# Optimization experiments

Measured on AMD Instinct MI355X. Metric: run time of the kernel, lower is better.

The kernel has to match this reference:

```python
import jax, jax.numpy as jnp
import numpy as np

N_NODES = 100000
N_EDGES = 3200000
D_IN = 512
D_OUT = 256


def setup_inputs() -> dict:
    key = jax.random.key(0)
    k1, k2, k3, k4, k5 = jax.random.split(key, 5)
    x = jax.random.normal(k1, (N_NODES, D_IN), dtype=jnp.float32)
    edge_row = jax.random.randint(k2, (N_EDGES,), 0, N_NODES, dtype=jnp.int32)
    edge_col = jax.random.randint(k3, (N_EDGES,), 0, N_NODES, dtype=jnp.int32)
    edge_vals = jax.random.uniform(k4, (N_EDGES,), dtype=jnp.float32)
    # glorot uniform for W, zeros for bias (as in the torch module)
    init_range = float(np.sqrt(6.0 / (D_IN + D_OUT)))
    W = jax.random.uniform(k5, (D_IN, D_OUT), minval=-init_range, maxval=init_range, dtype=jnp.float32)
    b = jnp.zeros((D_OUT,), dtype=jnp.float32)
    return {"x": x, "edge_row": edge_row, "edge_col": edge_col,
            "edge_vals": edge_vals, "W": W, "b": b}


def reference(x, edge_row, edge_col, edge_vals, W, b):
    # dropout p=0 -> identity; feature transform
    pre_sup = x @ W                                   # [N, D_OUT]
    # SpMM: out[i] = sum_{e: row[e]==i} vals[e] * pre_sup[col[e]]
    gathered = pre_sup[edge_col] * edge_vals[:, None]  # [E, D_OUT]
    agg = jax.ops.segment_sum(gathered, edge_row, num_segments=N_NODES)
    out = agg + b
    # F.normalize(p=2, dim=0): L2-normalize each column over the node dim
    col_norm = jnp.sqrt(jnp.sum(out * out, axis=0, keepdims=True))
    out = out / jnp.maximum(col_norm, 1e-12)
    return jax.nn.softplus(out)
```

## Files before the change

### kernel.cpp

```cpp
#include <hip/hip_runtime.h>
#include <math.h>

#define N_NODES 100000
#define N_EDGES 3200000
#define D_IN 512
#define D_OUT 256
#define NBUK 391
#define LDA 40

typedef unsigned short ushort_t;
typedef unsigned int uint_t;

using f32x4 = __attribute__((ext_vector_type(4))) float;
using s16x8 = __attribute__((ext_vector_type(8))) short;

__device__ __forceinline__ ushort_t f2bf(float f) {
    union { float f; uint_t u; } v; v.f = f;
    uint_t r = v.u + 0x7FFFu + ((v.u >> 16) & 1u);
    return (ushort_t)(r >> 16);
}
__device__ __forceinline__ float bf2f(uint_t u) {
    union { uint_t u; float f; } v; v.u = u << 16;
    return v.f;
}

__global__ __launch_bounds__(256) void cvt_w(const float* __restrict__ W,
                                             ushort_t* __restrict__ Wt) {
    int idx = blockIdx.x * 256 + threadIdx.x;
    int k = idx >> 8, n = idx & 255;
    Wt[(size_t)n * D_IN + k] = f2bf(W[idx]);
}

__global__ __launch_bounds__(256) void gemm_xw(const float* __restrict__ X,
                                               const ushort_t* __restrict__ Wt,
                                               ushort_t* __restrict__ P) {
    __shared__ ushort_t As[128 * LDA];
    __shared__ ushort_t Bs[128 * LDA];
    const int tid = threadIdx.x;
    const int n0 = blockIdx.x * 128;
    const int m0 = blockIdx.y * 128;
    const int wave = tid >> 6, lane = tid & 63;
    const int quad = lane >> 4, r16 = lane & 15;
    const int wm = (wave >> 1) * 64, wn = (wave & 1) * 64;

    f32x4 acc[4][4] = {};

    for (int k0 = 0; k0 < D_IN; k0 += 32) {
#pragma unroll
        for (int it = 0; it < 2; ++it) {
            int f = tid + it * 256;
            int row = f >> 2, kc = (f & 3) * 8;
            int grow = m0 + row;
            s16x8 av = {};
            if (grow < N_NODES) {
                const float* xp = X + (size_t)grow * D_IN + k0 + kc;
                f32x4 v0 = *(const f32x4*)(xp);
                f32x4 v1 = *(const f32x4*)(xp + 4);
                av[0] = (short)f2bf(v0[0]); av[1] = (short)f2bf(v0[1]);
                av[2] = (short)f2bf(v0[2]); av[3] = (short)f2bf(v0[3]);
                av[4] = (short)f2bf(v1[0]); av[5] = (short)f2bf(v1[1]);
                av[6] = (short)f2bf(v1[2]); av[7] = (short)f2bf(v1[3]);
            }
            *(s16x8*)(&As[row * LDA + kc]) = av;
            s16x8 bv = *(const s16x8*)(Wt + (size_t)(n0 + row) * D_IN + k0 + kc);
            *(s16x8*)(&Bs[row * LDA + kc]) = bv;
        }
        __syncthreads();

        s16x8 a[4], b[4];
#pragma unroll
        for (int i = 0; i < 4; ++i)
            a[i] = *(const s16x8*)(&As[(wm + i * 16 + r16) * LDA + quad * 8]);
#pragma unroll
        for (int j = 0; j < 4; ++j)
            b[j] = *(const s16x8*)(&Bs[(wn + j * 16 + r16) * LDA + quad * 8]);
#pragma unroll
        for (int i = 0; i < 4; ++i)
#pragma unroll
            for (int j = 0; j < 4; ++j)
                acc[i][j] = __builtin_amdgcn_mfma_f32_16x16x32_bf16(a[i], b[j], acc[i][j], 0, 0, 0);
        __syncthreads();
    }

#pragma unroll
    for (int i = 0; i < 4; ++i) {
#pragma unroll
        for (int rr = 0; rr < 4; ++rr) {
            int grow = m0 + wm + i * 16 + quad * 4 + rr;
            if (grow >= N_NODES) continue;
#pragma unroll
            for (int j = 0; j < 4; ++j) {
                int gcol = n0 + wn + j * 16 + r16;
                P[(size_t)grow * D_OUT + gcol] = f2bf(acc[i][j][rr]);
            }
        }
    }
}

__global__ __launch_bounds__(256) void bhist(const int* __restrict__ erow,
                                             int* __restrict__ bcnt) {
    __shared__ int l[NBUK];
    for (int b = threadIdx.x; b < NBUK; b += 256) l[b] = 0;
    __syncthreads();
    int base = blockIdx.x * 4096;
#pragma unroll
    for (int i = 0; i < 16; ++i) {
        int e = base + i * 256 + threadIdx.x;
        if (e < N_EDGES) atomicAdd(&l[erow[e] >> 8], 1);
    }
    __syncthreads();
    for (int b = threadIdx.x; b < NBUK; b += 256)
        if (l[b]) atomicAdd(&bcnt[b], l[b]);
}

__global__ void bscan(const int* __restrict__ bcnt, int* __restrict__ bbase,
                      int* __restrict__ bcursor, int* __restrict__ rstart) {
    __shared__ int sc[512];
    int t = threadIdx.x;
    int v = (t < NBUK) ? bcnt[t] : 0;
    sc[t] = v;
    __syncthreads();
    for (int off = 1; off < 512; off <<= 1) {
        int x = (t >= off) ? sc[t - off] : 0;
        __syncthreads();
        sc[t] += x;
        __syncthreads();
    }
    if (t < NBUK) { int excl = sc[t] - v; bbase[t] = excl; bcursor[t] = excl; }
    if (t == 0) { bbase[NBUK] = N_EDGES; rstart[N_NODES] = N_EDGES; }
}

__global__ __launch_bounds__(256) void bucket_scatter(const int* __restrict__ erow,
                                                      const int* __restrict__ ecol,
                                                      const float* __restrict__ eval,
                                                      int* __restrict__ bcursor,
                                                      uint2* __restrict__ bkt) {
    __shared__ int lcnt[NBUK];
    __shared__ int lbase[NBUK];
    const int t = threadIdx.x;
    for (int b = t; b < NBUK; b += 256) lcnt[b] = 0;
    __syncthreads();
    const int base = blockIdx.x * 4096;
#pragma unroll
    for (int i = 0; i < 16; ++i) {
        int e = base + i * 256 + t;
        if (e < N_EDGES) atomicAdd(&lcnt[erow[e] >> 8], 1);
    }
    __syncthreads();
    for (int b = t; b < NBUK; b += 256) {
        int c = lcnt[b];
        if (c) lbase[b] = atomicAdd(&bcursor[b], c);
        lcnt[b] = 0;
    }
    __syncthreads();
#pragma unroll
    for (int i = 0; i < 16; ++i) {
        int e = base + i * 256 + t;
        if (e < N_EDGES) {
            int r = erow[e];
            int b = r >> 8;
            int off = atomicAdd(&lcnt[b], 1);
            uint2 p;
            p.x = ((uint_t)(r & 255) << 17) | (uint_t)ecol[e];
            p.y = __float_as_uint(eval[e]);
            bkt[lbase[b] + off] = p;
        }
    }
}

__global__ __launch_bounds__(256) void csr_build(const uint2* __restrict__ bkt,
                                                 const int* __restrict__ bbase,
                                                 int* __restrict__ rstart,
                                                 uint2* __restrict__ csr) {
    __shared__ int hcnt[256];
    __shared__ int sc[256];
    __shared__ int cur[256];
    const int t = threadIdx.x, b = blockIdx.x;
    const int beg = bbase[b], end = bbase[b + 1];
    hcnt[t] = 0;
    __syncthreads();
    for (int i = beg + t; i < end; i += 256)
        atomicAdd(&hcnt[bkt[i].x >> 17], 1);
    __syncthreads();
    int v = hcnt[t];
    sc[t] = v;
    __syncthreads();
    for (int off = 1; off < 256; off <<= 1) {
        int x = (t >= off) ? sc[t - off] : 0;
        __syncthreads();
        sc[t] += x;
        __syncthreads();
    }
    int excl = sc[t] - v;
    int row = b * 256 + t;
    if (row < N_NODES) rstart[row] = beg + excl;
    cur[t] = excl;
    __syncthreads();
    for (int i = beg + t; i < end; i += 256) {
        uint2 u = bkt[i];
        int lr = u.x >> 17;
        int off = atomicAdd(&cur[lr], 1);
        uint2 o;
        o.x = u.x & 0x1FFFFu;
        o.y = u.y;
        csr[beg + off] = o;
    }
}

__global__ __launch_bounds__(64) void spmm_kernel(const uint2* __restrict__ csr,
                                                  const int* __restrict__ row_start,
                                                  const ushort_t* __restrict__ pre,
                                                  const float* __restrict__ bias,
                                                  float* __restrict__ out) {
    __shared__ uint2 epairs[64];
    const int node = blockIdx.x;
    const int lane = threadIdx.x;
    const int beg = row_start[node], end = row_start[node + 1];
    float a0 = 0.f, a1 = 0.f, a2 = 0.f, a3 = 0.f;
    for (int base = beg; base < end; base += 64) {
        int cnt = min(end - base, 64);
        if (lane < cnt) epairs[lane] = csr[base + lane];
        __syncthreads();
        for (int e = 0; e < cnt; ++e) {
            uint2 p = epairs[e];
            float w = __uint_as_float(p.y);
            const uint_t* rowp = (const uint_t*)(pre + (size_t)p.x * D_OUT);
            uint2 g = *(const uint2*)(rowp + lane * 2);
            a0 = fmaf(w, bf2f(g.x & 0xFFFFu), a0);
            a1 = fmaf(w, bf2f(g.x >> 16), a1);
            a2 = fmaf(w, bf2f(g.y & 0xFFFFu), a2);
            a3 = fmaf(w, bf2f(g.y >> 16), a3);
        }
        __syncthreads();
    }
    const float* b4 = bias + lane * 4;
    f32x4 o;
    o[0] = a0 + b4[0]; o[1] = a1 + b4[1]; o[2] = a2 + b4[2]; o[3] = a3 + b4[3];
    *(f32x4*)(out + (size_t)node * D_OUT + lane * 4) = o;
}

__global__ __launch_bounds__(256) void colsq_kernel(const float* __restrict__ out,
                                                    float* __restrict__ colsq) {
    const int f = threadIdx.x;
    float s = 0.f;
    for (int i = blockIdx.x; i < N_NODES; i += gridDim.x) {
        float v = out[(size_t)i * D_OUT + f];
        s = fmaf(v, v, s);
    }
    atomicAdd(&colsq[f], s);
}

__global__ __launch_bounds__(256) void finalize_kernel(float* __restrict__ out,
                                                       const float* __restrict__ colsq) {
    __shared__ float inv[256];
    const int t = threadIdx.x;
    float n = sqrtf(colsq[t]);
    inv[t] = 1.0f / fmaxf(n, 1e-12f);
    __syncthreads();
    const size_t total4 = (size_t)N_NODES * D_OUT / 4;
    for (size_t i = (size_t)blockIdx.x * 256 + t; i < total4; i += (size_t)gridDim.x * 256) {
        f32x4 v = ((const f32x4*)out)[i];
        int fbase = (int)((i * 4) & (D_OUT - 1));
        f32x4 o;
#pragma unroll
        for (int c = 0; c < 4; ++c) {
            float x = v[c] * inv[fbase + c];
            float tt = __expf(x);
            float y = __logf(1.0f + tt);
            o[c] = (x > 20.f) ? x : y;
        }
        ((f32x4*)out)[i] = o;
    }
}

extern "C" void kernel_launch(void* const* d_in, const int* in_sizes, int n_in,
                              void* d_out, int out_size, void* d_ws, size_t ws_size,
                              hipStream_t stream) {
    const float* x    = (const float*)d_in[0];
    const int*   erow = (const int*)d_in[1];
    const int*   ecol = (const int*)d_in[2];
    const float* eval = (const float*)d_in[3];
    const float* W    = (const float*)d_in[4];
    const float* b    = (const float*)d_in[5];
    float* out = (float*)d_out;
    char* ws = (char*)d_ws;

    uint2*    bkt     = (uint2*)   (ws + 0);
    ushort_t* pre     = (ushort_t*)(ws + 0);
    uint2*    csr     = (uint2*)   (ws + 51200000);
    int*      rstart  = (int*)     (ws + 76800000);
    float*    colsq   = (float*)   (ws + 77200016);
    int*      bcnt    = (int*)     (ws + 77201040);
    int*      bbase   = (int*)     (ws + 77202608);
    int*      bcursor = (int*)     (ws + 77204176);
    ushort_t* Wt      = (ushort_t*)(ws + 77205760);

    (void)hipMemsetAsync(bcnt, 0, NBUK * sizeof(int), stream);
    (void)hipMemsetAsync(colsq, 0, D_OUT * sizeof(float), stream);

    bhist<<<782, 256, 0, stream>>>(erow, bcnt);
    bscan<<<1, 512, 0, stream>>>(bcnt, bbase, bcursor, rstart);
    bucket_scatter<<<782, 256, 0, stream>>>(erow, ecol, eval, bcursor, bkt);
    csr_build<<<NBUK, 256, 0, stream>>>(bkt, bbase, rstart, csr);
    cvt_w<<<512, 256, 0, stream>>>(W, Wt);
    gemm_xw<<<dim3(2, 782), 256, 0, stream>>>(x, Wt, pre);
    spmm_kernel<<<N_NODES, 64, 0, stream>>>(csr, rstart, pre, b, out);
    colsq_kernel<<<512, 256, 0, stream>>>(out, colsq);
    finalize_kernel<<<1024, 256, 0, stream>>>(out, colsq);
}
```

Baseline: 866.0 us.

## Restructure SpMM: split wave into half-waves with 16-byte gathers and 4-edge unroll

The SpMM kernel now packs four nodes per 256-thread block, one wavefront per node. Each half-wave handles alternating edges, so a wave works on two edges at once. Each lane gathers 16 bytes (8 bf16 features) per edge, and four edges are issued together to keep more independent loads in flight. The half-wave partial sums are combined with a cross-lane shuffle before the bias add and store. The edge list in LDS is zero-padded (zero weight, node 0) so reads past the real edge count are harmless, but that wastes some gathers on nodes with few edges. Block-level barriers are dropped and the code relies on wavefront lockstep for its LDS reuse.

```diff
diff --git a/kernel.cpp b/kernel.cpp
--- a/kernel.cpp
+++ b/kernel.cpp
@@ -13,6 +13,7 @@
 
 using f32x4 = __attribute__((ext_vector_type(4))) float;
 using s16x8 = __attribute__((ext_vector_type(8))) short;
+using u32x4 = __attribute__((ext_vector_type(4))) uint_t;
 
 __device__ __forceinline__ ushort_t f2bf(float f) {
     union { float f; uint_t u; } v; v.f = f;
@@ -207,36 +208,104 @@
     }
 }
 
-__global__ __launch_bounds__(64) void spmm_kernel(const uint2* __restrict__ csr,
-                                                  const int* __restrict__ row_start,
-                                                  const ushort_t* __restrict__ pre,
-                                                  const float* __restrict__ bias,
-                                                  float* __restrict__ out) {
-    __shared__ uint2 epairs[64];
-    const int node = blockIdx.x;
-    const int lane = threadIdx.x;
+__global__ __launch_bounds__(256) void spmm_kernel(const uint2* __restrict__ csr,
+                                                   const int* __restrict__ row_start,
+                                                   const ushort_t* __restrict__ pre,
+                                                   const float* __restrict__ bias,
+                                                   float* __restrict__ out) {
+    __shared__ uint2 epairs[4][64];
+    const int wv   = threadIdx.x >> 6;
+    const int lane = threadIdx.x & 63;
+    const int half = lane >> 5;
+    const int l32  = lane & 31;
+    const int node = blockIdx.x * 4 + wv;
+
     const int beg = row_start[node], end = row_start[node + 1];
+
     float a0 = 0.f, a1 = 0.f, a2 = 0.f, a3 = 0.f;
+    float a4 = 0.f, a5 = 0.f, a6 = 0.f, a7 = 0.f;
+
     for (int base = beg; base < end; base += 64) {
-        int cnt = min(end - base, 64);
-        if (lane < cnt) epairs[lane] = csr[base + lane];
-        __syncthreads();
-        for (int e = 0; e < cnt; ++e) {
-            uint2 p = epairs[e];
-            float w = __uint_as_float(p.y);
-            const uint_t* rowp = (const uint_t*)(pre + (size_t)p.x * D_OUT);
-            uint2 g = *(const uint2*)(rowp + lane * 2);
-            a0 = fmaf(w, bf2f(g.x & 0xFFFFu), a0);
-            a1 = fmaf(w, bf2f(g.x >> 16), a1);
-            a2 = fmaf(w, bf2f(g.y & 0xFFFFu), a2);
-            a3 = fmaf(w, bf2f(g.y >> 16), a3);
-        }
-        __syncthreads();
-    }
-    const float* b4 = bias + lane * 4;
+        const int cnt = min(end - base, 64);
+        uint2 p0;
+        p0.x = 0u; p0.y = 0u;
+        if (lane < cnt) p0 = csr[base + lane];
+        epairs[wv][lane] = p0;
+
+        const int iters = (cnt + 7) >> 3;
+        for (int it = 0; it < iters; ++it) {
+            const int e0 = it * 8 + half;
+            uint2 q0 = epairs[wv][e0 + 0];
+            uint2 q1 = epairs[wv][e0 + 2];
+            uint2 q2 = epairs[wv][e0 + 4];
+            uint2 q3 = epairs[wv][e0 + 6];
+
+            u32x4 g0 = *(const u32x4*)(pre + (((size_t)q0.x) << 8) + l32 * 8);
+            u32x4 g1 = *(const u32x4*)(pre + (((size_t)q1.x) << 8) + l32 * 8);
+            u32x4 g2 = *(const u32x4*)(pre + (((size_t)q2.x) << 8) + l32 * 8);
+            u32x4 g3 = *(const u32x4*)(pre + (((size_t)q3.x) << 8) + l32 * 8);
+
+            const float w0 = __uint_as_float(q0.y);
+            const float w1 = __uint_as_float(q1.y);
+            const float w2 = __uint_as_float(q2.y);
+            const float w3 = __uint_as_float(q3.y);
+
+            a0 = fmaf(w0, bf2f(g0[0] & 0xFFFFu), a0);
+            a1 = fmaf(w0, bf2f(g0[0] >> 16),     a1);
+            a2 = fmaf(w0, bf2f(g0[1] & 0xFFFFu), a2);
+            a3 = fmaf(w0, bf2f(g0[1] >> 16),     a3);
+            a4 = fmaf(w0, bf2f(g0[2] & 0xFFFFu), a4);
+            a5 = fmaf(w0, bf2f(g0[2] >> 16),     a5);
+            a6 = fmaf(w0, bf2f(g0[3] & 0xFFFFu), a6);
+            a7 = fmaf(w0, bf2f(g0[3] >> 16),     a7);
+
+            a0 = fmaf(w1, bf2f(g1[0] & 0xFFFFu), a0);
+            a1 = fmaf(w1, bf2f(g1[0] >> 16),     a1);
+            a2 = fmaf(w1, bf2f(g1[1] & 0xFFFFu), a2);
+            a3 = fmaf(w1, bf2f(g1[1] >> 16),     a3);
+            a4 = fmaf(w1, bf2f(g1[2] & 0xFFFFu), a4);
+            a5 = fmaf(w1, bf2f(g1[2] >> 16),     a5);
+            a6 = fmaf(w1, bf2f(g1[3] & 0xFFFFu), a6);
+            a7 = fmaf(w1, bf2f(g1[3] >> 16),     a7);
+
+            a0 = fmaf(w2, bf2f(g2[0] & 0xFFFFu), a0);
+            a1 = fmaf(w2, bf2f(g2[0] >> 16),     a1);
+            a2 = fmaf(w2, bf2f(g2[1] & 0xFFFFu), a2);
+            a3 = fmaf(w2, bf2f(g2[1] >> 16),     a3);
+            a4 = fmaf(w2, bf2f(g2[2] & 0xFFFFu), a4);
+            a5 = fmaf(w2, bf2f(g2[2] >> 16),     a5);
+            a6 = fmaf(w2, bf2f(g2[3] & 0xFFFFu), a6);
+            a7 = fmaf(w2, bf2f(g2[3] >> 16),     a7);
+
+            a0 = fmaf(w3, bf2f(g3[0] & 0xFFFFu), a0);
+            a1 = fmaf(w3, bf2f(g3[0] >> 16),     a1);
+            a2 = fmaf(w3, bf2f(g3[1] & 0xFFFFu), a2);
+            a3 = fmaf(w3, bf2f(g3[1] >> 16),     a3);
+            a4 = fmaf(w3, bf2f(g3[2] & 0xFFFFu), a4);
+            a5 = fmaf(w3, bf2f(g3[2] >> 16),     a5);
+            a6 = fmaf(w3, bf2f(g3[3] & 0xFFFFu), a6);
+            a7 = fmaf(w3, bf2f(g3[3] >> 16),     a7);
+        }
+    }
+
+    a0 += __shfl_xor(a0, 32);
+    a1 += __shfl_xor(a1, 32);
+    a2 += __shfl_xor(a2, 32);
+    a3 += __shfl_xor(a3, 32);
+    a4 += __shfl_xor(a4, 32);
+    a5 += __shfl_xor(a5, 32);
+    a6 += __shfl_xor(a6, 32);
+    a7 += __shfl_xor(a7, 32);
+
+    const int fbase = l32 * 8 + half * 4;
+    const float* bp = bias + fbase;
+    float s0 = half ? a4 : a0;
+    float s1 = half ? a5 : a1;
+    float s2 = half ? a6 : a2;
+    float s3 = half ? a7 : a3;
     f32x4 o;
-    o[0] = a0 + b4[0]; o[1] = a1 + b4[1]; o[2] = a2 + b4[2]; o[3] = a3 + b4[3];
-    *(f32x4*)(out + (size_t)node * D_OUT + lane * 4) = o;
+    o[0] = s0 + bp[0]; o[1] = s1 + bp[1]; o[2] = s2 + bp[2]; o[3] = s3 + bp[3];
+    *(f32x4*)(out + (size_t)node * D_OUT + fbase) = o;
 }
 
 __global__ __launch_bounds__(256) void colsq_kernel(const float* __restrict__ out,
@@ -304,7 +373,7 @@
     csr_build<<<NBUK, 256, 0, stream>>>(bkt, bbase, rstart, csr);
     cvt_w<<<512, 256, 0, stream>>>(W, Wt);
     gemm_xw<<<dim3(2, 782), 256, 0, stream>>>(x, Wt, pre);
-    spmm_kernel<<<N_NODES, 64, 0, stream>>>(csr, rstart, pre, b, out);
+    spmm_kernel<<<N_NODES / 4, 256, 0, stream>>>(csr, rstart, pre, b, out);
     colsq_kernel<<<512, 256, 0, stream>>>(out, colsq);
     finalize_kernel<<<1024, 256, 0, stream>>>(out, colsq);
 }
```

Measured after the change: 869.2 us. About the same (+0.4%).
